# Performance work log

Hardware: AMD Instinct MI355X
Metric: run time of the kernel (lower is better)

Reference implementation:

```python
import jax, jax.numpy as jnp
import numpy as np

NE, NM, D = 10000, 2048, 128
LEVELS = 6  # levels arg 5 -> self.levels = 6 relation types


def setup_inputs() -> dict:
    key = jax.random.key(0)
    ks = jax.random.split(key, 9)
    s = 0.05
    return {
        "emb_entity": jax.random.normal(ks[0], (1, NE, D), jnp.float32),
        "emb_mole": jax.random.normal(ks[1], (1, NM, D), jnp.float32),
        "entity_mole_weight": jax.random.uniform(ks[2], (NE, NM), jnp.float32),
        "W1": jax.random.normal(ks[3], (LEVELS, D, D), jnp.float32) * s,
        "root1": jax.random.normal(ks[4], (D, D), jnp.float32) * s,
        "b1": jax.random.normal(ks[5], (D,), jnp.float32) * s,
        "W2": jax.random.normal(ks[6], (LEVELS, D, D), jnp.float32) * s,
        "root2": jax.random.normal(ks[7], (D, D), jnp.float32) * s,
        "b2": jax.random.normal(ks[8], (D,), jnp.float32) * s,
    }


def reference(emb_entity, emb_mole, entity_mole_weight, W1, root1, b1, W2, root2, b2):
    x_e = emb_entity[0]  # [NE, D]
    x_m = emb_mole[0]    # [NM, D]
    # weight w in (i/LEVELS, (i+1)/LEVELS]  <=>  ceil(w*LEVELS) - 1 == i ; only i=1..LEVELS-1 form edges
    lev = jnp.ceil(entity_mole_weight * LEVELS).astype(jnp.int32) - 1  # [NE, NM]

    def rel_agg(x_src, W):
        # RGCN mean aggregation per relation type (edges Mole -> Entity), summed over relations
        out = jnp.zeros((x_e.shape[0], W.shape[-1]), x_src.dtype)
        for r in range(1, LEVELS):
            mask = (lev == r).astype(x_src.dtype)          # [NE, NM] relation-r adjacency
            cnt = mask.sum(axis=1, keepdims=True)          # in-degree per entity for relation r
            inv = jnp.where(cnt > 0, 1.0 / cnt, 0.0)
            out = out + ((mask @ x_src) * inv) @ W[r]      # mean message then relation transform
        return out

    # conv1 over homogeneous graph [Entity; Mole]; moles receive no edges -> root+bias only
    e1 = x_e @ root1 + rel_agg(x_m, W1) + b1
    m1 = x_m @ root1 + b1
    e1 = jax.nn.relu(e1)
    m1 = jax.nn.relu(m1)
    # conv2; only the entity slice of the output is returned
    e2 = e1 @ root2 + rel_agg(m1, W2) + b2
    return e2[None]  # [1, NE, D]
```

## Files before the change

### kernel.cpp

```cpp
#include <hip/hip_runtime.h>
#include <stdint.h>


#define NE 10000
#define NM 2048
#define NEPAD 10112
#define MB64 158
#define KSPLIT 8

typedef short bf8_t __attribute__((ext_vector_type(8)));
typedef float f16f  __attribute__((ext_vector_type(16)));

__device__ __forceinline__ uint16_t f2bf(float f){
  uint32_t u = __float_as_uint(f);
  u += 0x7FFFu + ((u >> 16) & 1u);
  return (uint16_t)(u >> 16);
}

__device__ __forceinline__ f16f mfma32(bf8_t a, bf8_t b, f16f c){
  return __builtin_amdgcn_mfma_f32_32x32x16_bf16(a, b, c, 0, 0, 0);
}

__global__ __launch_bounds__(256) void k_init(
    const float* __restrict__ root1, const float* __restrict__ root2,
    const float* __restrict__ W1, const float* __restrict__ W2,
    uint16_t* __restrict__ r1t, uint16_t* __restrict__ r2t,
    uint16_t* __restrict__ w1t, uint16_t* __restrict__ w2t,
    const float* __restrict__ w, const float* __restrict__ xe,
    uint32_t* __restrict__ levq, float* __restrict__ inv,
    uint16_t* __restrict__ xebf){
  int t = threadIdx.x;
  if (blockIdx.x < 48){
    int idx = blockIdx.x*4096 + t;
    #pragma unroll
    for (int it = 0; it < 16; it++, idx += 256){
      int slab = idx >> 14;
      int pos  = idx & 16383;
      int d = pos >> 7, k = pos & 127;
      float v; uint16_t* dst;
      if (slab == 0)      { v = root1[k*128 + d]; dst = r1t; }
      else if (slab == 1) { v = root2[k*128 + d]; dst = r2t; }
      else if (slab < 7)  { v = W1[(slab-1)*16384 + k*128 + d]; dst = w1t + (slab-2)*16384; }
      else                { v = W2[(slab-6)*16384 + k*128 + d]; dst = w2t + (slab-7)*16384; }
      dst[pos] = f2bf(v);
    }
    return;
  }
  int brow = (blockIdx.x - 48) * 32;
  int rloc = t >> 3, p = t & 7;
  int row = brow + rloc;
  bool active = row < NE;
  const float* wr = w + (size_t)row * NM;
  unsigned long long cnt = 0ull;
  __shared__ uint32_t tile[32][33];

  for (int cp = 0; cp < 8; cp++){
    uint32_t packs[4];
    #pragma unroll
    for (int q = 0; q < 4; q++){
      int gck = cp*32 + p + 8*q;
      uint32_t L = 0;
      if (active){
        const float4* f = (const float4*)(wr + gck*8);
        float4 f0 = f[0], f1 = f[1];
        float wv[8] = {f0.x,f0.y,f0.z,f0.w, f1.x,f1.y,f1.z,f1.w};
        #pragma unroll
        for (int e = 0; e < 8; e++){
          int s = (int)ceilf(wv[e]*6.0f);
          if (s >= 2) cnt += 1ull << (12*(s-2));
          L |= (uint32_t)s << (4*e);
        }
      }
      packs[q] = L;
    }
    __syncthreads();
    #pragma unroll
    for (int q = 0; q < 4; q++) tile[p + 8*q][rloc] = packs[q];
    __syncthreads();
    int ckk = t >> 3;
    int r4  = (t & 7) * 4;
    size_t base = (size_t)(cp*32 + ckk) * NEPAD + brow + r4;
    *(uint4*)(levq + base) = make_uint4(tile[ckk][r4], tile[ckk][r4+1],
                                        tile[ckk][r4+2], tile[ckk][r4+3]);
  }

  unsigned long long c = cnt;
  c += __shfl_xor(c, 1);
  c += __shfl_xor(c, 2);
  c += __shfl_xor(c, 4);
  if (p == 0 && row < NEPAD){
    if (active){
      inv[row*8 + 0] = 0.f; inv[row*8 + 6] = 0.f; inv[row*8 + 7] = 0.f;
      #pragma unroll
      for (int r = 1; r <= 5; r++){
        uint32_t cc = (uint32_t)((c >> (12*(r-1))) & 0xFFFull);
        inv[row*8 + r] = cc ? 1.0f/(float)cc : 0.f;
      }
    } else {
      #pragma unroll
      for (int i = 0; i < 8; i++) inv[row*8 + i] = 0.f;
    }
  }

  int f0i = p * 16;
  if (active){
    union { uint16_t u[16]; uint4 q[2]; } ub;
    #pragma unroll
    for (int j = 0; j < 4; j++){
      float4 a = *(const float4*)(xe + (size_t)row*128 + f0i + j*4);
      ub.u[j*4+0]=f2bf(a.x); ub.u[j*4+1]=f2bf(a.y); ub.u[j*4+2]=f2bf(a.z); ub.u[j*4+3]=f2bf(a.w);
    }
    *(uint4*)(xebf + (size_t)row*128 + f0i)     = ub.q[0];
    *(uint4*)(xebf + (size_t)row*128 + f0i + 8) = ub.q[1];
  } else if (row < NEPAD){
    uint4 z = make_uint4(0,0,0,0);
    *(uint4*)(xebf + (size_t)row*128 + f0i)     = z;
    *(uint4*)(xebf + (size_t)row*128 + f0i + 8) = z;
  }
}

__global__ __launch_bounds__(256) void k_gemm(
    const float* __restrict__ Af, const uint16_t* __restrict__ Bm,
    const uint16_t* __restrict__ Bz, const float* __restrict__ bias,
    uint16_t* __restrict__ m1out, uint16_t* __restrict__ zpk){
  int tid = threadIdx.x;
  int lane = tid & 63, wid = tid >> 6;
  int l31 = lane & 31, g = lane >> 5;
  int by = blockIdx.y;
  bool m1path = (by == 0);
  int r = by - 1;
  const uint16_t* B = m1path ? Bm : (Bz + (size_t)r*16384);
  int arow = blockIdx.x*128 + wid*32 + l31;

  f16f acc[4];
  #pragma unroll
  for (int n = 0; n < 4; n++)
    #pragma unroll
    for (int i = 0; i < 16; i++) acc[n][i] = 0.f;

  #pragma unroll
  for (int ksI = 0; ksI < 8; ksI++){
    int k0 = ksI*16 + g*8;
    const float* ap = Af + (size_t)arow*128 + k0;
    float4 f0 = *(const float4*)ap;
    float4 f1 = *(const float4*)(ap + 4);
    union { uint16_t u[8]; bf8_t v; } ua;
    ua.u[0]=f2bf(f0.x); ua.u[1]=f2bf(f0.y); ua.u[2]=f2bf(f0.z); ua.u[3]=f2bf(f0.w);
    ua.u[4]=f2bf(f1.x); ua.u[5]=f2bf(f1.y); ua.u[6]=f2bf(f1.z); ua.u[7]=f2bf(f1.w);
    #pragma unroll
    for (int n = 0; n < 4; n++){
      bf8_t b = *(const bf8_t*)(B + (size_t)(n*32 + l31)*128 + k0);
      acc[n] = mfma32(ua.v, b, acc[n]);
    }
  }
  #pragma unroll
  for (int n = 0; n < 4; n++){
    int colg = n*32 + l31;
    float bv = m1path ? bias[colg] : 0.f;
    #pragma unroll
    for (int v = 0; v < 16; v++){
      int rowl = (v&3) + 8*(v>>2) + 4*g;
      int rg = blockIdx.x*128 + wid*32 + rowl;
      float val = acc[n][v];
      if (m1path){
        m1out[(size_t)rg*128 + colg] = f2bf(fmaxf(val + bv, 0.f));
      } else {
        int pos = ((rg & 1) << 2) | ((rg & 7) >> 1);
        zpk[(size_t)(r*256 + (rg>>3))*1024 + colg*8 + pos] = f2bf(val);
      }
    }
  }
}

template<int NSLAB, bool FUSE>
__global__ __launch_bounds__(128, 2) void k_conv(
    const uint32_t* __restrict__ levq, const float* __restrict__ inv,
    const uint16_t* __restrict__ zpk, const uint16_t* __restrict__ aroot,
    const uint16_t* __restrict__ rt,
    const uint16_t* __restrict__ gA, const uint16_t* __restrict__ gB,
    uint16_t* __restrict__ gOut,
    uint16_t* __restrict__ p16, float* __restrict__ p32){
  int tid = threadIdx.x;
  int lane = tid & 63, wid = tid >> 6;
  int l31 = lane & 31, g = lane >> 5;

  if (FUSE && blockIdx.x >= MB64){
    int b = blockIdx.y*20 + (blockIdx.x - MB64);
    int r = b >> 5;
    int rowb = (b & 31)*64 + wid*32;
    int arow = rowb + l31;
    const uint16_t* B = gB + (size_t)r*16384;
    f16f acc[4];
    #pragma unroll
    for (int n = 0; n < 4; n++)
      #pragma unroll
      for (int i = 0; i < 16; i++) acc[n][i] = 0.f;
    #pragma unroll
    for (int ksI = 0; ksI < 8; ksI++){
      int k0 = ksI*16 + g*8;
      bf8_t a = *(const bf8_t*)(gA + (size_t)arow*128 + k0);
      #pragma unroll
      for (int n = 0; n < 4; n++){
        bf8_t bb = *(const bf8_t*)(B + (size_t)(n*32 + l31)*128 + k0);
        acc[n] = mfma32(a, bb, acc[n]);
      }
    }
    #pragma unroll
    for (int n = 0; n < 4; n++){
      int colg = n*32 + l31;
      #pragma unroll
      for (int v = 0; v < 16; v++){
        int rowl = (v&3) + 8*(v>>2) + 4*g;
        int rg = rowb + rowl;
        int pos = ((rg & 1) << 2) | ((rg & 7) >> 1);
        gOut[(size_t)(r*256 + (rg>>3))*1024 + colg*8 + pos] = f2bf(acc[n][v]);
      }
    }
    return;
  }

  int brow = blockIdx.x*64;
  int ks = blockIdx.y;
  int kc0 = ks*32;
  int wn = wid;

  __shared__ uint16_t stage[2][10240];

  int row0 = brow + l31;
  int row1 = row0 + 32;

  uint32_t tlo[2][5], thi[2][5];
  #pragma unroll
  for (int mt = 0; mt < 2; mt++){
    int rg = mt ? row1 : row0;
    #pragma unroll
    for (int r = 1; r <= 5; r++){
      uint32_t bits = (uint32_t)f2bf(inv[(size_t)rg*8 + r]);
      int sh = 8*((r+1)&3);
      tlo[mt][r-1] = (bits & 0xFFu) << sh;
      thi[mt][r-1] = (bits >> 8)    << sh;
    }
  }

  f16f acc[2][2];
  #pragma unroll
  for (int a0=0;a0<2;a0++)
    #pragma unroll
    for (int b0=0;b0<2;b0++)
      #pragma unroll
      for (int i=0;i<16;i++) acc[a0][b0][i]=0.f;

  uint4 sreg[10];
  #pragma unroll
  for (int j = 0; j < 10; j++){
    int r = j >> 1, pc = j & 1;
    sreg[j] = *(const uint4*)(zpk + (size_t)(r*256 + kc0 + pc)*1024 + tid*8);
  }
  #pragma unroll
  for (int j = 0; j < 10; j++)
    *(uint4*)(&stage[0][j*1024 + tid*8]) = sreg[j];

  uint32_t Lc0 = levq[(size_t)(kc0 + g)*NEPAD + row0];
  uint32_t Lc1 = levq[(size_t)(kc0 + g)*NEPAD + row1];
  __syncthreads();

  int buf = 0;
  for (int kk = 0; kk < 16; kk++){
    uint32_t Ln0, Ln1;
    if (kk < 15){
      int ktn = kc0 + (kk+1)*2;
      #pragma unroll
      for (int j = 0; j < 10; j++){
        int r = j >> 1, pc = j & 1;
        sreg[j] = *(const uint4*)(zpk + (size_t)(r*256 + ktn + pc)*1024 + tid*8);
      }
      Ln0 = levq[(size_t)(ktn + g)*NEPAD + row0];
      Ln1 = levq[(size_t)(ktn + g)*NEPAD + row1];
    }
    uint32_t sx0 = Lc0 & 0x0F0F0F0Fu, sy0 = (Lc0 >> 4) & 0x0F0F0F0Fu;
    uint32_t sx1 = Lc1 & 0x0F0F0F0Fu, sy1 = (Lc1 >> 4) & 0x0F0F0F0Fu;
    const uint16_t* sb = &stage[buf][g*1024 + l31*8];
    #pragma unroll
    for (int r = 1; r <= 5; r++){
      bf8_t bn0 = *(const bf8_t*)(sb + (r-1)*2048 + (wn*2  )*256);
      bf8_t bn1 = *(const bf8_t*)(sb + (r-1)*2048 + (wn*2+1)*256);
      #pragma unroll
      for (int mt = 0; mt < 2; mt++){
        uint32_t sx = mt ? sx1 : sx0;
        uint32_t sy = mt ? sy1 : sy0;
        uint32_t TL = tlo[mt][r-1], TH = thi[mt][r-1];
        uint32_t pl, ph, ql, qh;
        if (r < 3){
          pl = __builtin_amdgcn_perm(0u, TL, sx);
          ph = __builtin_amdgcn_perm(0u, TH, sx);
          ql = __builtin_amdgcn_perm(0u, TL, sy);
          qh = __builtin_amdgcn_perm(0u, TH, sy);
        } else {
          pl = __builtin_amdgcn_perm(TL, 0u, sx);
          ph = __builtin_amdgcn_perm(TH, 0u, sx);
          ql = __builtin_amdgcn_perm(TL, 0u, sy);
          qh = __builtin_amdgcn_perm(TH, 0u, sy);
        }
        union { uint32_t u[4]; bf8_t v; } A;
        A.u[0] = __builtin_amdgcn_perm(ph, pl, 0x05010400u);
        A.u[1] = __builtin_amdgcn_perm(ph, pl, 0x07030602u);
        A.u[2] = __builtin_amdgcn_perm(qh, ql, 0x05010400u);
        A.u[3] = __builtin_amdgcn_perm(qh, ql, 0x07030602u);
        acc[mt][0] = mfma32(A.v, bn0, acc[mt][0]);
        acc[mt][1] = mfma32(A.v, bn1, acc[mt][1]);
      }
    }
    if (kk < 15){
      #pragma unroll
      for (int j = 0; j < 10; j++)
        *(uint4*)(&stage[buf^1][j*1024 + tid*8]) = sreg[j];
      __syncthreads();
      buf ^= 1;
      Lc0 = Ln0; Lc1 = Ln1;
    }
  }

  {
    int k0 = ks*16 + g*8;
    bf8_t a0 = *(const bf8_t*)(aroot + (size_t)row0*128 + k0);
    bf8_t a1 = *(const bf8_t*)(aroot + (size_t)row1*128 + k0);
    #pragma unroll
    for (int nt = 0; nt < 2; nt++){
      bf8_t rb = *(const bf8_t*)(rt + (size_t)((wn*2+nt)*32 + l31)*128 + k0);
      acc[0][nt] = mfma32(a0, rb, acc[0][nt]);
      acc[1][nt] = mfma32(a1, rb, acc[1][nt]);
    }
  }

  if (NSLAB == 8){
    uint16_t* dst = p16 + (size_t)ks*NEPAD*128;
    #pragma unroll
    for (int mt = 0; mt < 2; mt++){
      #pragma unroll
      for (int nt = 0; nt < 2; nt++){
        int colg = (wn*2+nt)*32 + l31;
        #pragma unroll
        for (int v = 0; v < 16; v++){
          int rowl = (v&3) + 8*(v>>2) + 4*g;
          dst[(size_t)(brow + mt*32 + rowl)*128 + colg] = f2bf(acc[mt][nt][v]);
        }
      }
    }
  } else {
    #pragma unroll
    for (int mt = 0; mt < 2; mt++){
      #pragma unroll
      for (int nt = 0; nt < 2; nt++){
        int colg = (wn*2+nt)*32 + l31;
        #pragma unroll
        for (int v = 0; v < 16; v++){
          int rowl = (v&3) + 8*(v>>2) + 4*g;
          unsafeAtomicAdd(&p32[(size_t)(brow + mt*32 + rowl)*128 + colg],
                          acc[mt][nt][v]);
        }
      }
    }
  }
}

template<bool C1, bool S16>
__global__ __launch_bounds__(256) void k_red(
    const uint16_t* __restrict__ p16, const float* __restrict__ p32,
    const float* __restrict__ bias, uint16_t* __restrict__ e1bf,
    float* __restrict__ out){
  size_t idx8 = ((size_t)blockIdx.x*256 + threadIdx.x) * 8;
  int col = (int)(idx8 & 127);
  float s[8];
  #pragma unroll
  for (int j = 0; j < 8; j++) s[j] = bias[col + j];
  if (S16){
    #pragma unroll
    for (int sl = 0; sl < 8; sl++){
      union { uint4 q; uint16_t h[8]; } u;
      u.q = *(const uint4*)(p16 + (size_t)sl*NEPAD*128 + idx8);
      #pragma unroll
      for (int j = 0; j < 8; j++) s[j] += __uint_as_float(((uint32_t)u.h[j]) << 16);
    }
  } else {
    #pragma unroll
    for (int j = 0; j < 8; j += 4){
      float4 v = *(const float4*)(p32 + idx8 + j);
      s[j] += v.x; s[j+1] += v.y; s[j+2] += v.z; s[j+3] += v.w;
    }
  }
  if (C1){
    union { uint16_t u[8]; uint4 q; } ub;
    #pragma unroll
    for (int j = 0; j < 8; j++) ub.u[j] = f2bf(fmaxf(s[j], 0.f));
    *(uint4*)(e1bf + idx8) = ub.q;
  } else {
    if (idx8 < (size_t)NE*128){
      *(float4*)(out + idx8)     = make_float4(s[0], s[1], s[2], s[3]);
      *(float4*)(out + idx8 + 4) = make_float4(s[4], s[5], s[6], s[7]);
    }
  }
}

extern "C" void kernel_launch(void* const* d_in, const int* in_sizes, int n_in,
                              void* d_out, int out_size, void* d_ws, size_t ws_size,
                              hipStream_t stream){
  const float* xe  = (const float*)d_in[0];
  const float* xm  = (const float*)d_in[1];
  const float* w   = (const float*)d_in[2];
  const float* W1  = (const float*)d_in[3];
  const float* r1  = (const float*)d_in[4];
  const float* b1  = (const float*)d_in[5];
  const float* W2  = (const float*)d_in[6];
  const float* r2  = (const float*)d_in[7];
  const float* b2  = (const float*)d_in[8];
  float* out = (float*)d_out;
  char* ws = (char*)d_ws;

  constexpr size_t OFF_INV  = 0;
  constexpr size_t OFF_XEBF = OFF_INV  + (size_t)NEPAD*8*4;
  constexpr size_t OFF_M1   = OFF_XEBF + (size_t)NEPAD*128*2;
  constexpr size_t OFF_Z1   = OFF_M1   + (size_t)NM*128*2;
  constexpr size_t OFF_Z2   = OFF_Z1   + (size_t)5*NM*128*2;
  constexpr size_t OFF_R1T  = OFF_Z2   + (size_t)5*NM*128*2;
  constexpr size_t OFF_R2T  = OFF_R1T  + 128*128*2;
  constexpr size_t OFF_W1T  = OFF_R2T  + 128*128*2;
  constexpr size_t OFF_W2T  = OFF_W1T  + (size_t)5*128*128*2;
  constexpr size_t OFF_LEVQ = OFF_W2T  + (size_t)5*128*128*2;
  constexpr size_t OFF_PART = OFF_LEVQ + (size_t)256*NEPAD*4;
  constexpr size_t SLAB16   = (size_t)NEPAD*128*2;
  constexpr size_t NEED_A   = OFF_PART + 8*SLAB16;
  constexpr size_t SLABF    = (size_t)NEPAD*128*4;

  float*    inv  = (float*)   (ws + OFF_INV);
  uint16_t* xebf = (uint16_t*)(ws + OFF_XEBF);
  uint16_t* m1   = (uint16_t*)(ws + OFF_M1);
  uint16_t* z1   = (uint16_t*)(ws + OFF_Z1);
  uint16_t* z2   = (uint16_t*)(ws + OFF_Z2);
  uint16_t* r1t  = (uint16_t*)(ws + OFF_R1T);
  uint16_t* r2t  = (uint16_t*)(ws + OFF_R2T);
  uint16_t* w1t  = (uint16_t*)(ws + OFF_W1T);
  uint16_t* w2t  = (uint16_t*)(ws + OFF_W2T);
  uint32_t* levq = (uint32_t*)(ws + OFF_LEVQ);
  uint16_t* p16  = (uint16_t*)(ws + OFF_PART);
  float*    p32  = (float*)   (ws + OFF_PART);

  bool tierA = (ws_size >= NEED_A);

  hipLaunchKernelGGL(k_init, dim3(48 + NEPAD/32), dim3(256), 0, stream,
                     r1, r2, W1, W2, r1t, r2t, w1t, w2t,
                     w, xe, levq, inv, xebf);
  hipLaunchKernelGGL(k_gemm, dim3(16,6), dim3(256), 0, stream,
                     xm, r1t, w1t, b1, m1, z1);
  if (tierA){
    hipLaunchKernelGGL((k_conv<8,true>), dim3(MB64 + 20, KSPLIT), dim3(128), 0, stream,
                       levq, inv, z1, xebf, r1t, m1, w2t, z2, p16, (float*)nullptr);
    hipLaunchKernelGGL((k_red<true,true>), dim3(NEPAD*128/2048), dim3(256), 0, stream,
                       p16, (const float*)nullptr, b1, xebf, (float*)nullptr);
    hipLaunchKernelGGL((k_conv<8,false>), dim3(MB64, KSPLIT), dim3(128), 0, stream,
                       levq, inv, z2, xebf, r2t,
                       (const uint16_t*)nullptr, (const uint16_t*)nullptr,
                       (uint16_t*)nullptr, p16, (float*)nullptr);
    hipLaunchKernelGGL((k_red<false,true>), dim3(NEPAD*128/2048), dim3(256), 0, stream,
                       p16, (const float*)nullptr, b2, (uint16_t*)nullptr, out);
  } else {
    hipMemsetAsync(p32, 0, SLABF, stream);
    hipLaunchKernelGGL((k_conv<1,true>), dim3(MB64 + 20, KSPLIT), dim3(128), 0, stream,
                       levq, inv, z1, xebf, r1t, m1, w2t, z2,
                       (uint16_t*)nullptr, p32);
    hipLaunchKernelGGL((k_red<true,false>), dim3(NEPAD*128/2048), dim3(256), 0, stream,
                       (const uint16_t*)nullptr, p32, b1, xebf, (float*)nullptr);
    hipMemsetAsync(p32, 0, SLABF, stream);
    hipLaunchKernelGGL((k_conv<1,false>), dim3(MB64, KSPLIT), dim3(128), 0, stream,
                       levq, inv, z2, xebf, r2t,
                       (const uint16_t*)nullptr, (const uint16_t*)nullptr,
                       (uint16_t*)nullptr, (uint16_t*)nullptr, p32);
    hipLaunchKernelGGL((k_red<false,false>), dim3(NEPAD*128/2048), dim3(256), 0, stream,
                       (const uint16_t*)nullptr, p32, b2, (uint16_t*)nullptr, out);
  }
}
```

Before: 132.6 us.

## Enlarge conv tile to 128 rows with four waves each owning full N

The conv kernel moves from 64-row blocks of 2 waves (each wave 2x2 MFMA tiles) to 128-row blocks of 4 waves, where each wave owns 32 rows and all 128 output columns. The staged Z slab in shared memory is now shared by twice as many rows, halving global reloads of the slab per output row, and the expansion of levels into A fragments happens once per row instead of being split across waves. The fused z2-GEMM tail is remapped to 10 extra blocks of 128 rows. The cost is fewer blocks (79x8) and higher register pressure per wave with four accumulators, under launch bounds of 256 threads and 3 blocks per CU.

```diff
diff --git a/kernel.cpp b/kernel.cpp
--- a/kernel.cpp
+++ b/kernel.cpp
@@ -5,7 +5,7 @@
 #define NE 10000
 #define NM 2048
 #define NEPAD 10112
-#define MB64 158
+#define MB128 79
 #define KSPLIT 8
 
 typedef short bf8_t __attribute__((ext_vector_type(8)));
@@ -173,7 +173,7 @@
 }
 
 template<int NSLAB, bool FUSE>
-__global__ __launch_bounds__(128, 2) void k_conv(
+__global__ __launch_bounds__(256, 3) void k_conv(
     const uint32_t* __restrict__ levq, const float* __restrict__ inv,
     const uint16_t* __restrict__ zpk, const uint16_t* __restrict__ aroot,
     const uint16_t* __restrict__ rt,
@@ -184,10 +184,10 @@
   int lane = tid & 63, wid = tid >> 6;
   int l31 = lane & 31, g = lane >> 5;
 
-  if (FUSE && blockIdx.x >= MB64){
-    int b = blockIdx.y*20 + (blockIdx.x - MB64);
-    int r = b >> 5;
-    int rowb = (b & 31)*64 + wid*32;
+  if (FUSE && blockIdx.x >= MB128){
+    int b = blockIdx.y*10 + (blockIdx.x - MB128);
+    int r = b >> 4;
+    int rowb = (b & 15)*128 + wid*32;
     int arow = rowb + l31;
     const uint16_t* B = gB + (size_t)r*16384;
     f16f acc[4];
@@ -219,145 +219,125 @@
     return;
   }
 
-  int brow = blockIdx.x*64;
+  int brow = blockIdx.x*128;
   int ks = blockIdx.y;
   int kc0 = ks*32;
-  int wn = wid;
+  int row = brow + wid*32 + l31;
 
   __shared__ uint16_t stage[2][10240];
 
-  int row0 = brow + l31;
-  int row1 = row0 + 32;
-
-  uint32_t tlo[2][5], thi[2][5];
-  #pragma unroll
-  for (int mt = 0; mt < 2; mt++){
-    int rg = mt ? row1 : row0;
-    #pragma unroll
-    for (int r = 1; r <= 5; r++){
-      uint32_t bits = (uint32_t)f2bf(inv[(size_t)rg*8 + r]);
-      int sh = 8*((r+1)&3);
-      tlo[mt][r-1] = (bits & 0xFFu) << sh;
-      thi[mt][r-1] = (bits >> 8)    << sh;
-    }
-  }
-
-  f16f acc[2][2];
-  #pragma unroll
-  for (int a0=0;a0<2;a0++)
-    #pragma unroll
-    for (int b0=0;b0<2;b0++)
-      #pragma unroll
-      for (int i=0;i<16;i++) acc[a0][b0][i]=0.f;
-
-  uint4 sreg[10];
-  #pragma unroll
-  for (int j = 0; j < 10; j++){
-    int r = j >> 1, pc = j & 1;
-    sreg[j] = *(const uint4*)(zpk + (size_t)(r*256 + kc0 + pc)*1024 + tid*8);
-  }
-  #pragma unroll
-  for (int j = 0; j < 10; j++)
-    *(uint4*)(&stage[0][j*1024 + tid*8]) = sreg[j];
-
-  uint32_t Lc0 = levq[(size_t)(kc0 + g)*NEPAD + row0];
-  uint32_t Lc1 = levq[(size_t)(kc0 + g)*NEPAD + row1];
+  uint32_t tlo[5], thi[5];
+  #pragma unroll
+  for (int r = 1; r <= 5; r++){
+    uint32_t bits = (uint32_t)f2bf(inv[(size_t)row*8 + r]);
+    int sh = 8*((r+1)&3);
+    tlo[r-1] = (bits & 0xFFu) << sh;
+    thi[r-1] = (bits >> 8)    << sh;
+  }
+
+  f16f acc[4];
+  #pragma unroll
+  for (int n = 0; n < 4; n++)
+    #pragma unroll
+    for (int i = 0; i < 16; i++) acc[n][i] = 0.f;
+
+  uint4 sreg[5];
+  #pragma unroll
+  for (int j = 0; j < 5; j++){
+    int idx = j*256 + tid;
+    sreg[j] = *(const uint4*)(zpk + (size_t)((idx>>8)*256 + kc0 + ((idx>>7)&1))*1024
+                                   + (idx & 127)*8);
+  }
+  #pragma unroll
+  for (int j = 0; j < 5; j++)
+    *(uint4*)(&stage[0][(j*256 + tid)*8]) = sreg[j];
+
+  uint32_t Lc = levq[(size_t)(kc0 + g)*NEPAD + row];
   __syncthreads();
 
   int buf = 0;
   for (int kk = 0; kk < 16; kk++){
-    uint32_t Ln0, Ln1;
+    uint32_t Ln;
     if (kk < 15){
       int ktn = kc0 + (kk+1)*2;
       #pragma unroll
-      for (int j = 0; j < 10; j++){
-        int r = j >> 1, pc = j & 1;
-        sreg[j] = *(const uint4*)(zpk + (size_t)(r*256 + ktn + pc)*1024 + tid*8);
-      }
-      Ln0 = levq[(size_t)(ktn + g)*NEPAD + row0];
-      Ln1 = levq[(size_t)(ktn + g)*NEPAD + row1];
-    }
-    uint32_t sx0 = Lc0 & 0x0F0F0F0Fu, sy0 = (Lc0 >> 4) & 0x0F0F0F0Fu;
-    uint32_t sx1 = Lc1 & 0x0F0F0F0Fu, sy1 = (Lc1 >> 4) & 0x0F0F0F0Fu;
+      for (int j = 0; j < 5; j++){
+        int idx = j*256 + tid;
+        sreg[j] = *(const uint4*)(zpk + (size_t)((idx>>8)*256 + ktn + ((idx>>7)&1))*1024
+                                       + (idx & 127)*8);
+      }
+      Ln = levq[(size_t)(ktn + g)*NEPAD + row];
+    }
+    uint32_t sx = Lc & 0x0F0F0F0Fu, sy = (Lc >> 4) & 0x0F0F0F0Fu;
     const uint16_t* sb = &stage[buf][g*1024 + l31*8];
     #pragma unroll
     for (int r = 1; r <= 5; r++){
-      bf8_t bn0 = *(const bf8_t*)(sb + (r-1)*2048 + (wn*2  )*256);
-      bf8_t bn1 = *(const bf8_t*)(sb + (r-1)*2048 + (wn*2+1)*256);
-      #pragma unroll
-      for (int mt = 0; mt < 2; mt++){
-        uint32_t sx = mt ? sx1 : sx0;
-        uint32_t sy = mt ? sy1 : sy0;
-        uint32_t TL = tlo[mt][r-1], TH = thi[mt][r-1];
-        uint32_t pl, ph, ql, qh;
-        if (r < 3){
-          pl = __builtin_amdgcn_perm(0u, TL, sx);
-          ph = __builtin_amdgcn_perm(0u, TH, sx);
-          ql = __builtin_amdgcn_perm(0u, TL, sy);
-          qh = __builtin_amdgcn_perm(0u, TH, sy);
-        } else {
-          pl = __builtin_amdgcn_perm(TL, 0u, sx);
-          ph = __builtin_amdgcn_perm(TH, 0u, sx);
-          ql = __builtin_amdgcn_perm(TL, 0u, sy);
-          qh = __builtin_amdgcn_perm(TH, 0u, sy);
-        }
-        union { uint32_t u[4]; bf8_t v; } A;
-        A.u[0] = __builtin_amdgcn_perm(ph, pl, 0x05010400u);
-        A.u[1] = __builtin_amdgcn_perm(ph, pl, 0x07030602u);
-        A.u[2] = __builtin_amdgcn_perm(qh, ql, 0x05010400u);
-        A.u[3] = __builtin_amdgcn_perm(qh, ql, 0x07030602u);
-        acc[mt][0] = mfma32(A.v, bn0, acc[mt][0]);
-        acc[mt][1] = mfma32(A.v, bn1, acc[mt][1]);
-      }
+      bf8_t bn0 = *(const bf8_t*)(sb + (r-1)*2048);
+      bf8_t bn1 = *(const bf8_t*)(sb + (r-1)*2048 + 256);
+      bf8_t bn2 = *(const bf8_t*)(sb + (r-1)*2048 + 512);
+      bf8_t bn3 = *(const bf8_t*)(sb + (r-1)*2048 + 768);
+      uint32_t TL = tlo[r-1], TH = thi[r-1];
+      uint32_t pl, ph, ql, qh;
+      if (r < 3){
+        pl = __builtin_amdgcn_perm(0u, TL, sx);
+        ph = __builtin_amdgcn_perm(0u, TH, sx);
+        ql = __builtin_amdgcn_perm(0u, TL, sy);
+        qh = __builtin_amdgcn_perm(0u, TH, sy);
+      } else {
+        pl = __builtin_amdgcn_perm(TL, 0u, sx);
+        ph = __builtin_amdgcn_perm(TH, 0u, sx);
+        ql = __builtin_amdgcn_perm(TL, 0u, sy);
+        qh = __builtin_amdgcn_perm(TH, 0u, sy);
+      }
+      union { uint32_t u[4]; bf8_t v; } A;
+      A.u[0] = __builtin_amdgcn_perm(ph, pl, 0x05010400u);
+      A.u[1] = __builtin_amdgcn_perm(ph, pl, 0x07030602u);
+      A.u[2] = __builtin_amdgcn_perm(qh, ql, 0x05010400u);
+      A.u[3] = __builtin_amdgcn_perm(qh, ql, 0x07030602u);
+      acc[0] = mfma32(A.v, bn0, acc[0]);
+      acc[1] = mfma32(A.v, bn1, acc[1]);
+      acc[2] = mfma32(A.v, bn2, acc[2]);
+      acc[3] = mfma32(A.v, bn3, acc[3]);
     }
     if (kk < 15){
       #pragma unroll
-      for (int j = 0; j < 10; j++)
-        *(uint4*)(&stage[buf^1][j*1024 + tid*8]) = sreg[j];
+      for (int j = 0; j < 5; j++)
+        *(uint4*)(&stage[buf^1][(j*256 + tid)*8]) = sreg[j];
       __syncthreads();
       buf ^= 1;
-      Lc0 = Ln0; Lc1 = Ln1;
+      Lc = Ln;
     }
   }
 
   {
     int k0 = ks*16 + g*8;
-    bf8_t a0 = *(const bf8_t*)(aroot + (size_t)row0*128 + k0);
-    bf8_t a1 = *(const bf8_t*)(aroot + (size_t)row1*128 + k0);
-    #pragma unroll
-    for (int nt = 0; nt < 2; nt++){
-      bf8_t rb = *(const bf8_t*)(rt + (size_t)((wn*2+nt)*32 + l31)*128 + k0);
-      acc[0][nt] = mfma32(a0, rb, acc[0][nt]);
-      acc[1][nt] = mfma32(a1, rb, acc[1][nt]);
+    bf8_t a = *(const bf8_t*)(aroot + (size_t)row*128 + k0);
+    #pragma unroll
+    for (int nt = 0; nt < 4; nt++){
+      bf8_t rb = *(const bf8_t*)(rt + (size_t)(nt*32 + l31)*128 + k0);
+      acc[nt] = mfma32(a, rb, acc[nt]);
     }
   }
 
   if (NSLAB == 8){
     uint16_t* dst = p16 + (size_t)ks*NEPAD*128;
     #pragma unroll
-    for (int mt = 0; mt < 2; mt++){
-      #pragma unroll
-      for (int nt = 0; nt < 2; nt++){
-        int colg = (wn*2+nt)*32 + l31;
-        #pragma unroll
-        for (int v = 0; v < 16; v++){
-          int rowl = (v&3) + 8*(v>>2) + 4*g;
-          dst[(size_t)(brow + mt*32 + rowl)*128 + colg] = f2bf(acc[mt][nt][v]);
-        }
+    for (int nt = 0; nt < 4; nt++){
+      int colg = nt*32 + l31;
+      #pragma unroll
+      for (int v = 0; v < 16; v++){
+        int rowl = (v&3) + 8*(v>>2) + 4*g;
+        dst[(size_t)(brow + wid*32 + rowl)*128 + colg] = f2bf(acc[nt][v]);
       }
     }
   } else {
     #pragma unroll
-    for (int mt = 0; mt < 2; mt++){
-      #pragma unroll
-      for (int nt = 0; nt < 2; nt++){
-        int colg = (wn*2+nt)*32 + l31;
-        #pragma unroll
-        for (int v = 0; v < 16; v++){
-          int rowl = (v&3) + 8*(v>>2) + 4*g;
-          unsafeAtomicAdd(&p32[(size_t)(brow + mt*32 + rowl)*128 + colg],
-                          acc[mt][nt][v]);
-        }
+    for (int nt = 0; nt < 4; nt++){
+      int colg = nt*32 + l31;
+      #pragma unroll
+      for (int v = 0; v < 16; v++){
+        int rowl = (v&3) + 8*(v>>2) + 4*g;
+        unsafeAtomicAdd(&p32[(size_t)(brow + wid*32 + rowl)*128 + colg], acc[nt][v]);
       }
     }
   }
@@ -452,11 +432,11 @@
   hipLaunchKernelGGL(k_gemm, dim3(16,6), dim3(256), 0, stream,
                      xm, r1t, w1t, b1, m1, z1);
   if (tierA){
-    hipLaunchKernelGGL((k_conv<8,true>), dim3(MB64 + 20, KSPLIT), dim3(128), 0, stream,
+    hipLaunchKernelGGL((k_conv<8,true>), dim3(MB128 + 10, KSPLIT), dim3(256), 0, stream,
                        levq, inv, z1, xebf, r1t, m1, w2t, z2, p16, (float*)nullptr);
     hipLaunchKernelGGL((k_red<true,true>), dim3(NEPAD*128/2048), dim3(256), 0, stream,
                        p16, (const float*)nullptr, b1, xebf, (float*)nullptr);
-    hipLaunchKernelGGL((k_conv<8,false>), dim3(MB64, KSPLIT), dim3(128), 0, stream,
+    hipLaunchKernelGGL((k_conv<8,false>), dim3(MB128, KSPLIT), dim3(256), 0, stream,
                        levq, inv, z2, xebf, r2t,
                        (const uint16_t*)nullptr, (const uint16_t*)nullptr,
                        (uint16_t*)nullptr, p16, (float*)nullptr);
@@ -464,13 +444,13 @@
                        p16, (const float*)nullptr, b2, (uint16_t*)nullptr, out);
   } else {
     hipMemsetAsync(p32, 0, SLABF, stream);
-    hipLaunchKernelGGL((k_conv<1,true>), dim3(MB64 + 20, KSPLIT), dim3(128), 0, stream,
+    hipLaunchKernelGGL((k_conv<1,true>), dim3(MB128 + 10, KSPLIT), dim3(256), 0, stream,
                        levq, inv, z1, xebf, r1t, m1, w2t, z2,
                        (uint16_t*)nullptr, p32);
     hipLaunchKernelGGL((k_red<true,false>), dim3(NEPAD*128/2048), dim3(256), 0, stream,
                        (const uint16_t*)nullptr, p32, b1, xebf, (float*)nullptr);
     hipMemsetAsync(p32, 0, SLABF, stream);
-    hipLaunchKernelGGL((k_conv<1,false>), dim3(MB64, KSPLIT), dim3(128), 0, stream,
+    hipLaunchKernelGGL((k_conv<1,false>), dim3(MB128, KSPLIT), dim3(256), 0, stream,
                        levq, inv, z2, xebf, r2t,
                        (const uint16_t*)nullptr, (const uint16_t*)nullptr,
                        (uint16_t*)nullptr, (uint16_t*)nullptr, p32);
```

Result: faster. 121.1 us (-8.7%).

## Drop LDS staging in k_conv and widen block tile to 128 rows

Applied to the files above, without the earlier changes.

The conv kernel no longer stages the packed relation-transformed mole features through double-buffered shared memory with barriers. Each wave now reads its B fragments directly from global/L2 and computes all 128 output columns for 64 rows, so a block covers 128 rows and the grid shrinks to 79 row-blocks. This removes LDS traffic and __syncthreads stalls but loses software prefetching and cross-wave reuse of B. It also doubles accumulator registers per wave and may lower occupancy.

```diff
diff --git a/kernel.cpp b/kernel.cpp
--- a/kernel.cpp
+++ b/kernel.cpp
@@ -5,7 +5,7 @@
 #define NE 10000
 #define NM 2048
 #define NEPAD 10112
-#define MB64 158
+#define MB128 79
 #define KSPLIT 8
 
 typedef short bf8_t __attribute__((ext_vector_type(8)));
@@ -184,8 +184,8 @@
   int lane = tid & 63, wid = tid >> 6;
   int l31 = lane & 31, g = lane >> 5;
 
-  if (FUSE && blockIdx.x >= MB64){
-    int b = blockIdx.y*20 + (blockIdx.x - MB64);
+  if (FUSE && blockIdx.x >= MB128){
+    int b = blockIdx.y*20 + (blockIdx.x - MB128);
     int r = b >> 5;
     int rowb = (b & 31)*64 + wid*32;
     int arow = rowb + l31;
@@ -219,20 +219,16 @@
     return;
   }
 
-  int brow = blockIdx.x*64;
+  int brow = blockIdx.x*128;
   int ks = blockIdx.y;
   int kc0 = ks*32;
-  int wn = wid;
-
-  __shared__ uint16_t stage[2][10240];
-
-  int row0 = brow + l31;
-  int row1 = row0 + 32;
+  int rowA = brow + wid*64 + l31;
+  int rowB = rowA + 32;
 
   uint32_t tlo[2][5], thi[2][5];
   #pragma unroll
   for (int mt = 0; mt < 2; mt++){
-    int rg = mt ? row1 : row0;
+    int rg = mt ? rowB : rowA;
     #pragma unroll
     for (int r = 1; r <= 5; r++){
       uint32_t bits = (uint32_t)f2bf(inv[(size_t)rg*8 + r]);
@@ -242,52 +238,32 @@
     }
   }
 
-  f16f acc[2][2];
+  f16f acc[2][4];
   #pragma unroll
   for (int a0=0;a0<2;a0++)
     #pragma unroll
-    for (int b0=0;b0<2;b0++)
+    for (int b0=0;b0<4;b0++)
       #pragma unroll
       for (int i=0;i<16;i++) acc[a0][b0][i]=0.f;
 
-  uint4 sreg[10];
-  #pragma unroll
-  for (int j = 0; j < 10; j++){
-    int r = j >> 1, pc = j & 1;
-    sreg[j] = *(const uint4*)(zpk + (size_t)(r*256 + kc0 + pc)*1024 + tid*8);
-  }
-  #pragma unroll
-  for (int j = 0; j < 10; j++)
-    *(uint4*)(&stage[0][j*1024 + tid*8]) = sreg[j];
-
-  uint32_t Lc0 = levq[(size_t)(kc0 + g)*NEPAD + row0];
-  uint32_t Lc1 = levq[(size_t)(kc0 + g)*NEPAD + row1];
-  __syncthreads();
-
-  int buf = 0;
   for (int kk = 0; kk < 16; kk++){
-    uint32_t Ln0, Ln1;
-    if (kk < 15){
-      int ktn = kc0 + (kk+1)*2;
-      #pragma unroll
-      for (int j = 0; j < 10; j++){
-        int r = j >> 1, pc = j & 1;
-        sreg[j] = *(const uint4*)(zpk + (size_t)(r*256 + ktn + pc)*1024 + tid*8);
-      }
-      Ln0 = levq[(size_t)(ktn + g)*NEPAD + row0];
-      Ln1 = levq[(size_t)(ktn + g)*NEPAD + row1];
-    }
-    uint32_t sx0 = Lc0 & 0x0F0F0F0Fu, sy0 = (Lc0 >> 4) & 0x0F0F0F0Fu;
-    uint32_t sx1 = Lc1 & 0x0F0F0F0Fu, sy1 = (Lc1 >> 4) & 0x0F0F0F0Fu;
-    const uint16_t* sb = &stage[buf][g*1024 + l31*8];
+    int kt = kc0 + kk*2 + g;
+    uint32_t LA = levq[(size_t)kt*NEPAD + rowA];
+    uint32_t LB = levq[(size_t)kt*NEPAD + rowB];
+    uint32_t sxA = LA & 0x0F0F0F0Fu, syA = (LA >> 4) & 0x0F0F0F0Fu;
+    uint32_t sxB = LB & 0x0F0F0F0Fu, syB = (LB >> 4) & 0x0F0F0F0Fu;
+    const uint16_t* zb = zpk + (size_t)kt*1024 + l31*8;
     #pragma unroll
     for (int r = 1; r <= 5; r++){
-      bf8_t bn0 = *(const bf8_t*)(sb + (r-1)*2048 + (wn*2  )*256);
-      bf8_t bn1 = *(const bf8_t*)(sb + (r-1)*2048 + (wn*2+1)*256);
+      const uint16_t* zr = zb + (size_t)(r-1)*262144;
+      bf8_t bn0 = *(const bf8_t*)(zr);
+      bf8_t bn1 = *(const bf8_t*)(zr + 256);
+      bf8_t bn2 = *(const bf8_t*)(zr + 512);
+      bf8_t bn3 = *(const bf8_t*)(zr + 768);
       #pragma unroll
       for (int mt = 0; mt < 2; mt++){
-        uint32_t sx = mt ? sx1 : sx0;
-        uint32_t sy = mt ? sy1 : sy0;
+        uint32_t sx = mt ? sxB : sxA;
+        uint32_t sy = mt ? syB : syA;
         uint32_t TL = tlo[mt][r-1], TH = thi[mt][r-1];
         uint32_t pl, ph, ql, qh;
         if (r < 3){
@@ -308,25 +284,19 @@
         A.u[3] = __builtin_amdgcn_perm(qh, ql, 0x07030602u);
         acc[mt][0] = mfma32(A.v, bn0, acc[mt][0]);
         acc[mt][1] = mfma32(A.v, bn1, acc[mt][1]);
-      }
-    }
-    if (kk < 15){
-      #pragma unroll
-      for (int j = 0; j < 10; j++)
-        *(uint4*)(&stage[buf^1][j*1024 + tid*8]) = sreg[j];
-      __syncthreads();
-      buf ^= 1;
-      Lc0 = Ln0; Lc1 = Ln1;
+        acc[mt][2] = mfma32(A.v, bn2, acc[mt][2]);
+        acc[mt][3] = mfma32(A.v, bn3, acc[mt][3]);
+      }
     }
   }
 
   {
     int k0 = ks*16 + g*8;
-    bf8_t a0 = *(const bf8_t*)(aroot + (size_t)row0*128 + k0);
-    bf8_t a1 = *(const bf8_t*)(aroot + (size_t)row1*128 + k0);
-    #pragma unroll
-    for (int nt = 0; nt < 2; nt++){
-      bf8_t rb = *(const bf8_t*)(rt + (size_t)((wn*2+nt)*32 + l31)*128 + k0);
+    bf8_t a0 = *(const bf8_t*)(aroot + (size_t)rowA*128 + k0);
+    bf8_t a1 = *(const bf8_t*)(aroot + (size_t)rowB*128 + k0);
+    #pragma unroll
+    for (int nt = 0; nt < 4; nt++){
+      bf8_t rb = *(const bf8_t*)(rt + (size_t)(nt*32 + l31)*128 + k0);
       acc[0][nt] = mfma32(a0, rb, acc[0][nt]);
       acc[1][nt] = mfma32(a1, rb, acc[1][nt]);
     }
@@ -337,12 +307,12 @@
     #pragma unroll
     for (int mt = 0; mt < 2; mt++){
       #pragma unroll
-      for (int nt = 0; nt < 2; nt++){
-        int colg = (wn*2+nt)*32 + l31;
+      for (int nt = 0; nt < 4; nt++){
+        int colg = nt*32 + l31;
         #pragma unroll
         for (int v = 0; v < 16; v++){
           int rowl = (v&3) + 8*(v>>2) + 4*g;
-          dst[(size_t)(brow + mt*32 + rowl)*128 + colg] = f2bf(acc[mt][nt][v]);
+          dst[(size_t)(brow + wid*64 + mt*32 + rowl)*128 + colg] = f2bf(acc[mt][nt][v]);
         }
       }
     }
@@ -350,12 +320,12 @@
     #pragma unroll
     for (int mt = 0; mt < 2; mt++){
       #pragma unroll
-      for (int nt = 0; nt < 2; nt++){
-        int colg = (wn*2+nt)*32 + l31;
+      for (int nt = 0; nt < 4; nt++){
+        int colg = nt*32 + l31;
         #pragma unroll
         for (int v = 0; v < 16; v++){
           int rowl = (v&3) + 8*(v>>2) + 4*g;
-          unsafeAtomicAdd(&p32[(size_t)(brow + mt*32 + rowl)*128 + colg],
+          unsafeAtomicAdd(&p32[(size_t)(brow + wid*64 + mt*32 + rowl)*128 + colg],
                           acc[mt][nt][v]);
         }
       }
@@ -452,11 +422,11 @@
   hipLaunchKernelGGL(k_gemm, dim3(16,6), dim3(256), 0, stream,
                      xm, r1t, w1t, b1, m1, z1);
   if (tierA){
-    hipLaunchKernelGGL((k_conv<8,true>), dim3(MB64 + 20, KSPLIT), dim3(128), 0, stream,
+    hipLaunchKernelGGL((k_conv<8,true>), dim3(MB128 + 20, KSPLIT), dim3(128), 0, stream,
                        levq, inv, z1, xebf, r1t, m1, w2t, z2, p16, (float*)nullptr);
     hipLaunchKernelGGL((k_red<true,true>), dim3(NEPAD*128/2048), dim3(256), 0, stream,
                        p16, (const float*)nullptr, b1, xebf, (float*)nullptr);
-    hipLaunchKernelGGL((k_conv<8,false>), dim3(MB64, KSPLIT), dim3(128), 0, stream,
+    hipLaunchKernelGGL((k_conv<8,false>), dim3(MB128, KSPLIT), dim3(128), 0, stream,
                        levq, inv, z2, xebf, r2t,
                        (const uint16_t*)nullptr, (const uint16_t*)nullptr,
                        (uint16_t*)nullptr, p16, (float*)nullptr);
@@ -464,13 +434,13 @@
                        p16, (const float*)nullptr, b2, (uint16_t*)nullptr, out);
   } else {
     hipMemsetAsync(p32, 0, SLABF, stream);
-    hipLaunchKernelGGL((k_conv<1,true>), dim3(MB64 + 20, KSPLIT), dim3(128), 0, stream,
+    hipLaunchKernelGGL((k_conv<1,true>), dim3(MB128 + 20, KSPLIT), dim3(128), 0, stream,
                        levq, inv, z1, xebf, r1t, m1, w2t, z2,
                        (uint16_t*)nullptr, p32);
     hipLaunchKernelGGL((k_red<true,false>), dim3(NEPAD*128/2048), dim3(256), 0, stream,
                        (const uint16_t*)nullptr, p32, b1, xebf, (float*)nullptr);
     hipMemsetAsync(p32, 0, SLABF, stream);
-    hipLaunchKernelGGL((k_conv<1,false>), dim3(MB64, KSPLIT), dim3(128), 0, stream,
+    hipLaunchKernelGGL((k_conv<1,false>), dim3(MB128, KSPLIT), dim3(128), 0, stream,
                        levq, inv, z2, xebf, r2t,
                        (const uint16_t*)nullptr, (const uint16_t*)nullptr,
                        (uint16_t*)nullptr, (uint16_t*)nullptr, p32);
```

New measurement: 144.4 us. 8.8% more time.
